# Optimization experiments

Measured on AMD Instinct MI355X. Metric: run time of the kernel, lower is better.

The kernel has to match this reference:

```python
import jax, jax.numpy as jnp
import numpy as np
import math

B, T, C, H, D = 2, 2048, 768, 12, 64


def _rms_norm(x):
    # torch F.rms_norm with eps=None -> finfo(dtype).eps, no learned weight
    eps = jnp.finfo(x.dtype).eps
    return x * jax.lax.rsqrt(jnp.mean(x * x, axis=-1, keepdims=True) + eps)


def _apply_rotary(x, cos, sin):
    # nanochat rotary: split head_dim into halves
    d = x.shape[-1] // 2
    x1, x2 = x[..., :d], x[..., d:]
    return jnp.concatenate([x1 * cos + x2 * sin, -x1 * sin + x2 * cos], axis=-1)


def setup_inputs() -> dict:
    key = jax.random.key(0)
    ks = jax.random.split(key, 8)
    s = 0.02
    x = jax.random.normal(ks[0], (B, T, C), jnp.float32)
    cos = jax.random.normal(ks[1], (1, T, 1, D // 2), jnp.float32)
    sin = jax.random.normal(ks[2], (1, T, 1, D // 2), jnp.float32)
    Wq = jax.random.normal(ks[3], (C, C), jnp.float32) * s
    Wk = jax.random.normal(ks[4], (C, C), jnp.float32) * s
    Wv = jax.random.normal(ks[5], (C, C), jnp.float32) * s
    Wo = jax.random.normal(ks[6], (C, C), jnp.float32) * s
    beta = jnp.ones((H,), jnp.float32) * 0.5
    return {"x": x, "cos": cos, "sin": sin, "Wq": Wq, "Wk": Wk, "Wv": Wv, "Wo": Wo, "beta": beta}


def reference(x, cos, sin, Wq, Wk, Wv, Wo, beta):
    b, t, c = x.shape
    h = beta.shape[0]
    d = c // h
    q = (x @ Wq.T).reshape(b, t, h, d)
    k = (x @ Wk.T).reshape(b, t, h, d)
    v = (x @ Wv.T).reshape(b, t, h, d)
    q = _rms_norm(_apply_rotary(q, cos, sin)).transpose(0, 2, 1, 3)  # (B,H,T,D)
    k = _rms_norm(_apply_rotary(k, cos, sin)).transpose(0, 2, 1, 3)
    v = v.transpose(0, 2, 1, 3)
    # phase coherence: mean over RoPE frequencies of cos(position_diff * theta)
    pos = jnp.arange(t, dtype=jnp.float32)
    theta = 10000.0 ** (-jnp.arange(0, d, 2, dtype=jnp.float32) / d)  # (D/2,)
    pdiff = pos[None, :] - pos[:, None]  # (T,T); cos is even so orientation is irrelevant
    coh_base = jnp.mean(jnp.cos(pdiff[:, :, None] * theta), axis=-1)  # (T,T)
    coherence = 1.0 + beta[None, :, None, None] * coh_base[None, None, :, :]  # (1,H,T,T)
    scores = jnp.einsum('bhqd,bhkd->bhqk', q, k) / math.sqrt(d)
    scores = scores * coherence
    w = jax.nn.softmax(scores, axis=-1)
    causal = jnp.tril(jnp.ones((t, t), dtype=bool))
    w = w * causal[None, None, :, :]
    w = w / (jnp.sum(w, axis=-1, keepdims=True) + 1e-8)
    y = jnp.einsum('bhqk,bhkd->bhqd', w, v)
    y = y.transpose(0, 2, 1, 3).reshape(b, t, c)
    return y @ Wo.T
```

## Files before the change

kernel.cpp:

```cpp
#include <hip/hip_runtime.h>
#include <hip/hip_bf16.h>
#include <math.h>

#define B_ 2
#define T_ 2048
#define C_ 768
#define H_ 12
#define D_ 64

typedef __attribute__((ext_vector_type(8))) short short8;
typedef __attribute__((ext_vector_type(4))) float f32x4;
typedef __attribute__((ext_vector_type(16))) float f32x16;

template <bool V> struct BoolC { static constexpr bool value = V; };

__device__ inline unsigned short f2bf(float f) {
    unsigned int x = __float_as_uint(f);
    unsigned int r = x + 0x7FFFu + ((x >> 16) & 1u);
    return (unsigned short)(r >> 16);
}

__device__ __forceinline__ unsigned cvtpk(float lo, float hi) {
    unsigned r;
    asm("v_cvt_pk_bf16_f32 %0, %1, %2" : "=v"(r) : "v"(lo), "v"(hi));
    return r;
}

__device__ __forceinline__ void plswap(unsigned& a, unsigned& b) {
    asm volatile("v_permlane32_swap_b32 %0, %1" : "+v"(a), "+v"(b));
}

__device__ __forceinline__ void gll16(const void* g, void* l) {
    __builtin_amdgcn_global_load_lds(
        (const __attribute__((address_space(1))) unsigned int*)g,
        (__attribute__((address_space(3))) unsigned int*)l, 16, 0, 0);
}

__global__ __launch_bounds__(256) void convert_all_kernel(const float* __restrict__ x,
                                                          const float* __restrict__ Wq,
                                                          const float* __restrict__ Wk,
                                                          const float* __restrict__ Wv,
                                                          const float* __restrict__ Wo,
                                                          unsigned short* __restrict__ xb,
                                                          unsigned short* __restrict__ wqkv,
                                                          unsigned short* __restrict__ wob,
                                                          float* __restrict__ coh) {
    if (blockIdx.x >= 5376) {
        int dd = (blockIdx.x - 5376) * 256 + threadIdx.x;
        if (dd < T_) {
            float s = 0.f;
            for (int m = 0; m < 32; ++m) {
                float theta = powf(10000.f, -(float)m / 32.f);
                s += cosf((float)dd * theta);
            }
            coh[dd] = s * (1.f / 32.f);
        }
        return;
    }
    int i = blockIdx.x * 256 + threadIdx.x;
    float4 v;
    ushort4* d;
    if (i < 786432) {
        v = ((const float4*)x)[i];
        d = (ushort4*)xb + i;
    } else {
        int wI = i - 786432;
        int widx = wI / 147456;
        int off = wI - widx * 147456;
        const float* W = widx == 0 ? Wq : widx == 1 ? Wk : widx == 2 ? Wv : Wo;
        v = ((const float4*)W)[off];
        unsigned short* base = (widx == 3) ? wob : (wqkv + widx * 589824);
        d = (ushort4*)base + off;
    }
    ushort4 o;
    o.x = f2bf(v.x); o.y = f2bf(v.y); o.z = f2bf(v.z); o.w = f2bf(v.w);
    *d = o;
}

__global__ __launch_bounds__(256) void gemm_qkv_kernel(const unsigned short* __restrict__ xb,
                                                       const unsigned short* __restrict__ wqkv,
                                                       const float* __restrict__ cosb,
                                                       const float* __restrict__ sinb,
                                                       unsigned short* __restrict__ qbf,
                                                       unsigned short* __restrict__ kbf,
                                                       unsigned short* __restrict__ vt) {
    __shared__ unsigned short lA[128][32];
    __shared__ unsigned short lB[128][32];
    __shared__ unsigned short tr[4][64][72];

    int bm = blockIdx.x, tn = blockIdx.y;
    int tid = threadIdx.x;
    int w = tid >> 6, lane = tid & 63;
    int rc = lane & 15, kg = lane >> 4;
    int wr = w >> 1, wc = w & 1;

    const unsigned short* ga = xb + (size_t)(bm * 128 + w * 32 + (lane >> 2)) * 768 + (lane & 3) * 8;
    const unsigned short* gb = wqkv + (size_t)(tn * 128 + w * 32 + (lane >> 2)) * 768 + (lane & 3) * 8;
    unsigned short* la0 = &lA[w * 32][0];
    unsigned short* la1 = &lA[w * 32 + 16][0];
    unsigned short* lb0 = &lB[w * 32][0];
    unsigned short* lb1 = &lB[w * 32 + 16][0];

    f32x4 acc[4][4];
    #pragma unroll
    for (int i = 0; i < 4; ++i)
        #pragma unroll
        for (int j = 0; j < 4; ++j) acc[i][j] = (f32x4){0.f, 0.f, 0.f, 0.f};

    for (int k0 = 0; k0 < 768; k0 += 32) {
        gll16(ga + k0, la0);
        gll16(ga + k0 + 16 * 768, la1);
        gll16(gb + k0, lb0);
        gll16(gb + k0 + 16 * 768, lb1);
        __syncthreads();
        short8 aF[4], bF[4];
        #pragma unroll
        for (int ai = 0; ai < 4; ++ai) aF[ai] = *(const short8*)&lA[wr * 64 + ai * 16 + rc][kg * 8];
        #pragma unroll
        for (int bj = 0; bj < 4; ++bj) bF[bj] = *(const short8*)&lB[wc * 64 + bj * 16 + rc][kg * 8];
        #pragma unroll
        for (int ai = 0; ai < 4; ++ai)
            #pragma unroll
            for (int bj = 0; bj < 4; ++bj)
                acc[ai][bj] = __builtin_amdgcn_mfma_f32_16x16x32_bf16(aF[ai], bF[bj], acc[ai][bj], 0, 0, 0);
        __syncthreads();
    }

    int hg = tn * 2 + wc;
    int tensor = hg / 12;
    int h = hg % 12;

    if (tensor < 2) {
        float scale = tensor == 0 ? 0.125f : 1.0f;
        unsigned short* dst = (tensor == 0 ? qbf : kbf);
        #pragma unroll
        for (int ai = 0; ai < 4; ++ai) {
            #pragma unroll
            for (int rr = 0; rr < 4; ++rr) {
                int m = bm * 128 + wr * 64 + ai * 16 + kg * 4 + rr;
                int b = m >> 11, t = m & 2047;
                float c0 = cosb[t * 32 + rc], c1 = cosb[t * 32 + 16 + rc];
                float s0 = sinb[t * 32 + rc], s1 = sinb[t * 32 + 16 + rc];
                float x0 = acc[ai][0][rr], x1 = acc[ai][1][rr];
                float x2 = acc[ai][2][rr], x3 = acc[ai][3][rr];
                float o0 = x0 * c0 + x2 * s0;
                float o1 = x1 * c1 + x3 * s1;
                float o2 = -x0 * s0 + x2 * c0;
                float o3 = -x1 * s1 + x3 * c1;
                float ss = o0 * o0 + o1 * o1 + o2 * o2 + o3 * o3;
                ss += __shfl_xor(ss, 1); ss += __shfl_xor(ss, 2);
                ss += __shfl_xor(ss, 4); ss += __shfl_xor(ss, 8);
                float rn = rsqrtf(ss * (1.f / 64.f) + 1.1920929e-07f) * scale;
                unsigned short* dp = dst + (((size_t)b * H_ + h) * T_ + t) * 64;
                dp[rc]      = f2bf(o0 * rn);
                dp[16 + rc] = f2bf(o1 * rn);
                dp[32 + rc] = f2bf(o2 * rn);
                dp[48 + rc] = f2bf(o3 * rn);
            }
        }
    } else {
        #pragma unroll
        for (int ai = 0; ai < 4; ++ai)
            #pragma unroll
            for (int bj = 0; bj < 4; ++bj)
                #pragma unroll
                for (int rr = 0; rr < 4; ++rr)
                    tr[w][bj * 16 + rc][ai * 16 + kg * 4 + rr] = f2bf(acc[ai][bj][rr]);
    }
    __syncthreads();
    if (tensor == 2) {
        int m0 = bm * 128 + wr * 64;
        int b = m0 >> 11, t0 = m0 & 2047;
        int d = lane;
        unsigned short* gp = vt + (((size_t)b * H_ + h) * 64 + d) * T_ + t0;
        const uint4* src = (const uint4*)&tr[w][d][0];
        #pragma unroll
        for (int i = 0; i < 8; ++i) ((uint4*)gp)[i] = src[i];
    }
}

__global__ __launch_bounds__(256) void gemm_out_kernel(const unsigned short* __restrict__ A,
                                                       const unsigned short* __restrict__ Bw,
                                                       float* __restrict__ C) {
    __shared__ unsigned short lA[128][32];
    __shared__ unsigned short lB[128][32];
    int bm = blockIdx.x, tn = blockIdx.y;
    int tid = threadIdx.x;
    int w = tid >> 6, lane = tid & 63;
    int rc = lane & 15, kg = lane >> 4;
    int wr = w >> 1, wc = w & 1;

    const unsigned short* ga = A + (size_t)(bm * 128 + w * 32 + (lane >> 2)) * 768 + (lane & 3) * 8;
    const unsigned short* gb = Bw + (size_t)(tn * 128 + w * 32 + (lane >> 2)) * 768 + (lane & 3) * 8;
    unsigned short* la0 = &lA[w * 32][0];
    unsigned short* la1 = &lA[w * 32 + 16][0];
    unsigned short* lb0 = &lB[w * 32][0];
    unsigned short* lb1 = &lB[w * 32 + 16][0];

    f32x4 acc[4][4];
    #pragma unroll
    for (int i = 0; i < 4; ++i)
        #pragma unroll
        for (int j = 0; j < 4; ++j) acc[i][j] = (f32x4){0.f, 0.f, 0.f, 0.f};

    for (int k0 = 0; k0 < 768; k0 += 32) {
        gll16(ga + k0, la0);
        gll16(ga + k0 + 16 * 768, la1);
        gll16(gb + k0, lb0);
        gll16(gb + k0 + 16 * 768, lb1);
        __syncthreads();
        short8 aF[4], bF[4];
        #pragma unroll
        for (int ai = 0; ai < 4; ++ai) aF[ai] = *(const short8*)&lA[wr * 64 + ai * 16 + rc][kg * 8];
        #pragma unroll
        for (int bj = 0; bj < 4; ++bj) bF[bj] = *(const short8*)&lB[wc * 64 + bj * 16 + rc][kg * 8];
        #pragma unroll
        for (int ai = 0; ai < 4; ++ai)
            #pragma unroll
            for (int bj = 0; bj < 4; ++bj)
                acc[ai][bj] = __builtin_amdgcn_mfma_f32_16x16x32_bf16(aF[ai], bF[bj], acc[ai][bj], 0, 0, 0);
        __syncthreads();
    }

    #pragma unroll
    for (int ai = 0; ai < 4; ++ai)
        #pragma unroll
        for (int rr = 0; rr < 4; ++rr) {
            int m = bm * 128 + wr * 64 + ai * 16 + kg * 4 + rr;
            #pragma unroll
            for (int bj = 0; bj < 4; ++bj)
                C[(size_t)m * 768 + tn * 128 + wc * 64 + bj * 16 + rc] = acc[ai][bj][rr];
        }
}

__global__ __launch_bounds__(256) void attn_flash_kernel(const unsigned short* __restrict__ qbf,
                                                         const unsigned short* __restrict__ kbf,
                                                         const unsigned short* __restrict__ vt,
                                                         const float* __restrict__ coh,
                                                         const float* __restrict__ beta,
                                                         unsigned short* __restrict__ yb) {
    __shared__ unsigned short kT[2][64][64];
    __shared__ unsigned short vT[2][64][64];
    __shared__ float cfl[T_];

    int p = blockIdx.x;
    int xcd = p & 7, kk = p >> 3;
    int bl = kk >> 5, jsl = kk & 31;
    int bh = xcd * 3 + bl;
    int jj = (bl == 0) ? jsl : (bl == 1 ? (31 - jsl) : ((jsl * 5 + 3) & 31));
    int tq = 31 - jj;
    int b = bh / H_, h = bh % H_;

    int tid = threadIdx.x;
    int w = tid >> 6, lane = tid & 63;
    int qs = w >> 1, js = w & 1;
    int ql = lane & 31, hl = lane >> 5;

    float bv = beta[h];
    for (int i = tid; i < T_; i += 256)
        cfl[i] = (1.f + bv * coh[i]) * 1.4426950408889634f;

    int qb = tq * 64;
    const unsigned short* kb = kbf + (size_t)bh * T_ * 64;
    const unsigned short* vb = vt + (size_t)bh * 64 * T_;

    const unsigned short* qrow = qbf + ((size_t)bh * T_ + qb + qs * 32 + ql) * 64 + hl * 8;
    short8 qf[4];
    #pragma unroll
    for (int d = 0; d < 4; ++d) qf[d] = *(const short8*)(qrow + d * 16);

    f32x16 acc0, acc1;
    #pragma unroll
    for (int i = 0; i < 16; ++i) { acc0[i] = 0.f; acc1[i] = 0.f; }
    float z = 0.f;

    int Rk = js * 32 + ql;
    int kby[4];
    #pragma unroll
    for (int d = 0; d < 4; ++d) kby[d] = Rk * 128 + (((d * 2 + hl) ^ (Rk & 7)) << 4);
    int vby0[2], vby1[2];
    #pragma unroll
    for (int ks = 0; ks < 2; ++ks) {
        int Rv0 = ql, Rv1 = 32 + ql;
        vby0[ks] = Rv0 * 128 + (((js * 4 + ks * 2 + hl) ^ (Rv0 & 7)) << 4);
        vby1[ks] = Rv1 * 128 + (((js * 4 + ks * 2 + hl) ^ (Rv1 & 7)) << 4);
    }
    const char* kbase = (const char*)&kT[0][0][0];
    const char* vbase = (const char*)&vT[0][0][0];

    int rloc = lane >> 3;
    int gsw = ((lane & 7) ^ rloc) * 8;
    int r0 = w * 16;

    auto stage = [&](int buf, int tj) {
        gll16(kb + (size_t)(tj + r0 + rloc) * 64 + gsw,      &kT[buf][r0][0]);
        gll16(kb + (size_t)(tj + r0 + 8 + rloc) * 64 + gsw,  &kT[buf][r0 + 8][0]);
        gll16(vb + (size_t)(r0 + rloc) * T_ + tj + gsw,      &vT[buf][r0][0]);
        gll16(vb + (size_t)(r0 + 8 + rloc) * T_ + tj + gsw,  &vT[buf][r0 + 8][0]);
    };

    int qpos = qb + qs * 32 + ql;

    auto body = [&](int buf, int tj, auto maskc) {
        constexpr bool M = decltype(maskc)::value;
        f32x16 s;
        #pragma unroll
        for (int i = 0; i < 16; ++i) s[i] = 0.f;
        const char* kp = kbase + buf * 8192;
        __builtin_amdgcn_s_setprio(1);
        #pragma unroll
        for (int d = 0; d < 4; ++d) {
            short8 kf = *(const short8*)(kp + kby[d]);
            s = __builtin_amdgcn_mfma_f32_32x32x16_bf16(kf, qf[d], s, 0, 0, 0);
        }
        __builtin_amdgcn_s_setprio(0);
        int base = qpos - tj - js * 32 - 4 * hl;
        float e[16];
        #pragma unroll
        for (int r = 0; r < 16; ++r) {
            int dd = base - ((r & 3) + 8 * (r >> 2));
            if constexpr (M) {
                float ex = __builtin_amdgcn_exp2f(s[r] * cfl[dd < 0 ? 0 : dd]);
                e[r] = dd >= 0 ? ex : 0.f;
            } else {
                e[r] = __builtin_amdgcn_exp2f(s[r] * cfl[dd]);
            }
            z += e[r];
        }
        unsigned A0 = cvtpk(e[0], e[1]),  B0 = cvtpk(e[2], e[3]);
        unsigned C0 = cvtpk(e[4], e[5]),  D0 = cvtpk(e[6], e[7]);
        unsigned E0 = cvtpk(e[8], e[9]),  F0 = cvtpk(e[10], e[11]);
        unsigned G0 = cvtpk(e[12], e[13]), H0 = cvtpk(e[14], e[15]);
        plswap(A0, C0); plswap(B0, D0); plswap(E0, G0); plswap(F0, H0);
        union U { unsigned u[4]; short8 s8; };
        U p0, p1;
        p0.u[0] = A0; p0.u[1] = B0; p0.u[2] = C0; p0.u[3] = D0;
        p1.u[0] = E0; p1.u[1] = F0; p1.u[2] = G0; p1.u[3] = H0;
        const char* vp = vbase + buf * 8192;
        short8 v00 = *(const short8*)(vp + vby0[0]);
        short8 v01 = *(const short8*)(vp + vby0[1]);
        short8 v10 = *(const short8*)(vp + vby1[0]);
        short8 v11 = *(const short8*)(vp + vby1[1]);
        __builtin_amdgcn_s_setprio(1);
        acc0 = __builtin_amdgcn_mfma_f32_32x32x16_bf16(v00, p0.s8, acc0, 0, 0, 0);
        acc0 = __builtin_amdgcn_mfma_f32_32x32x16_bf16(v01, p1.s8, acc0, 0, 0, 0);
        acc1 = __builtin_amdgcn_mfma_f32_32x32x16_bf16(v10, p0.s8, acc1, 0, 0, 0);
        acc1 = __builtin_amdgcn_mfma_f32_32x32x16_bf16(v11, p1.s8, acc1, 0, 0, 0);
        __builtin_amdgcn_s_setprio(0);
    };

    int nt = tq + 1;
    stage(0, 0);
    __syncthreads();
    int cur = 0;
    for (int it = 0; it < nt - 1; ++it) {
        stage(cur ^ 1, (it + 1) * 64);
        body(cur, it * 64, BoolC<false>{});
        __syncthreads();
        cur ^= 1;
    }
    if (qs > js)      body(cur, (nt - 1) * 64, BoolC<false>{});
    else if (qs == js) body(cur, (nt - 1) * 64, BoolC<true>{});
    __syncthreads();

    z += __shfl_xor(z, 32);
    float* osc = (float*)&kT[0][0][0];
    float* zbuf = (float*)&vT[0][0][0];
    if (js == 0) {
        float* o = osc + qs * 2048;
        #pragma unroll
        for (int r = 0; r < 16; ++r) {
            o[r * 64 + lane] = acc0[r];
            o[(16 + r) * 64 + lane] = acc1[r];
        }
        if (lane < 32) zbuf[qs * 32 + ql] = z;
    }
    __syncthreads();
    if (js == 1) {
        float zt = z + zbuf[qs * 32 + ql];
        float invz = 1.f / zt;
        const float* o = osc + qs * 2048;
        #pragma unroll
        for (int r = 0; r < 16; ++r) {
            acc0[r] = (acc0[r] + o[r * 64 + lane]) * invz;
            acc1[r] = (acc1[r] + o[(16 + r) * 64 + lane]) * invz;
        }
        int t = qb + qs * 32 + ql;
        unsigned short* yp = yb + (((size_t)b * T_ + t) * H_ + h) * 64;
        #pragma unroll
        for (int g = 0; g < 4; ++g) {
            uint2 st0, st1;
            st0.x = cvtpk(acc0[g * 4 + 0], acc0[g * 4 + 1]);
            st0.y = cvtpk(acc0[g * 4 + 2], acc0[g * 4 + 3]);
            *(uint2*)(yp + g * 8 + 4 * hl) = st0;
            st1.x = cvtpk(acc1[g * 4 + 0], acc1[g * 4 + 1]);
            st1.y = cvtpk(acc1[g * 4 + 2], acc1[g * 4 + 3]);
            *(uint2*)(yp + 32 + g * 8 + 4 * hl) = st1;
        }
    }
}

extern "C" void kernel_launch(void* const* d_in, const int* in_sizes, int n_in,
                              void* d_out, int out_size, void* d_ws, size_t ws_size,
                              hipStream_t stream) {
    const float* x    = (const float*)d_in[0];
    const float* cosb = (const float*)d_in[1];
    const float* sinb = (const float*)d_in[2];
    const float* Wq   = (const float*)d_in[3];
    const float* Wk   = (const float*)d_in[4];
    const float* Wv   = (const float*)d_in[5];
    const float* Wo   = (const float*)d_in[6];
    const float* beta = (const float*)d_in[7];
    float* out = (float*)d_out;

    char* ws = (char*)d_ws;
    unsigned short* xb   = (unsigned short*)(ws + 0);
    unsigned short* wqkv = (unsigned short*)(ws + 6291456);
    unsigned short* wob  = (unsigned short*)(ws + 9830400);
    unsigned short* qbf  = (unsigned short*)(ws + 11010048);
    unsigned short* kbf  = (unsigned short*)(ws + 17301504);
    unsigned short* vt   = (unsigned short*)(ws + 23592960);
    unsigned short* yb   = (unsigned short*)(ws + 29884416);
    float*          coh  = (float*)(ws + 36175872);

    convert_all_kernel<<<5384, 256, 0, stream>>>(x, Wq, Wk, Wv, Wo, xb, wqkv, wob, coh);

    dim3 gq(32, 18);
    gemm_qkv_kernel<<<gq, 256, 0, stream>>>(xb, wqkv, cosb, sinb, qbf, kbf, vt);

    attn_flash_kernel<<<B_ * H_ * (T_ / 64), 256, 0, stream>>>(qbf, kbf, vt, coh, beta, yb);

    dim3 go(32, 6);
    gemm_out_kernel<<<go, 256, 0, stream>>>(yb, wob, out);
}
```

Baseline: 114.9 us.

## Double-buffer GEMM LDS staging with vmcnt waits and narrow output GEMM tiles

Both projection GEMMs now double-buffer their LDS tiles. The next K-slice is issued before computing the current one, using explicit vmcnt waits and raw barriers instead of full __syncthreads. The QKV kernel puts the staging buffers and the transpose scratch in a union so LDS use stays bounded. The output GEMM switches to 128x64 tiles with twice as many blocks to raise occupancy on the small grid. The attention loop also replaces __syncthreads with a partial vmcnt wait plus barrier so prefetches stay in flight. The main risk is getting the waitcnt counts wrong for the async global-to-LDS loads.

```diff
diff --git a/kernel.cpp b/kernel.cpp
--- a/kernel.cpp
+++ b/kernel.cpp
@@ -13,6 +13,9 @@
 typedef __attribute__((ext_vector_type(16))) float f32x16;
 
 template <bool V> struct BoolC { static constexpr bool value = V; };
+
+#define SBAR() do { asm volatile("" ::: "memory"); __builtin_amdgcn_s_barrier(); asm volatile("" ::: "memory"); } while (0)
+#define WAITVM(N) asm volatile("s_waitcnt vmcnt(" #N ")" ::: "memory")
 
 __device__ inline unsigned short f2bf(float f) {
     unsigned int x = __float_as_uint(f);
@@ -77,6 +80,11 @@
     *d = o;
 }
 
+union QkvSmem {
+    struct { unsigned short A[2][128][32]; unsigned short Bm[2][128][32]; } g;
+    unsigned short tr[4][64][72];
+};
+
 __global__ __launch_bounds__(256) void gemm_qkv_kernel(const unsigned short* __restrict__ xb,
                                                        const unsigned short* __restrict__ wqkv,
                                                        const float* __restrict__ cosb,
@@ -84,9 +92,7 @@
                                                        unsigned short* __restrict__ qbf,
                                                        unsigned short* __restrict__ kbf,
                                                        unsigned short* __restrict__ vt) {
-    __shared__ unsigned short lA[128][32];
-    __shared__ unsigned short lB[128][32];
-    __shared__ unsigned short tr[4][64][72];
+    __shared__ QkvSmem sm;
 
     int bm = blockIdx.x, tn = blockIdx.y;
     int tid = threadIdx.x;
@@ -96,10 +102,6 @@
 
     const unsigned short* ga = xb + (size_t)(bm * 128 + w * 32 + (lane >> 2)) * 768 + (lane & 3) * 8;
     const unsigned short* gb = wqkv + (size_t)(tn * 128 + w * 32 + (lane >> 2)) * 768 + (lane & 3) * 8;
-    unsigned short* la0 = &lA[w * 32][0];
-    unsigned short* la1 = &lA[w * 32 + 16][0];
-    unsigned short* lb0 = &lB[w * 32][0];
-    unsigned short* lb1 = &lB[w * 32 + 16][0];
 
     f32x4 acc[4][4];
     #pragma unroll
@@ -107,24 +109,40 @@
         #pragma unroll
         for (int j = 0; j < 4; ++j) acc[i][j] = (f32x4){0.f, 0.f, 0.f, 0.f};
 
-    for (int k0 = 0; k0 < 768; k0 += 32) {
-        gll16(ga + k0, la0);
-        gll16(ga + k0 + 16 * 768, la1);
-        gll16(gb + k0, lb0);
-        gll16(gb + k0 + 16 * 768, lb1);
-        __syncthreads();
+    auto stageg = [&](int buf, int k0) {
+        gll16(ga + k0, &sm.g.A[buf][w * 32][0]);
+        gll16(ga + k0 + 16 * 768, &sm.g.A[buf][w * 32 + 16][0]);
+        gll16(gb + k0, &sm.g.Bm[buf][w * 32][0]);
+        gll16(gb + k0 + 16 * 768, &sm.g.Bm[buf][w * 32 + 16][0]);
+    };
+    auto comp = [&](int buf) {
         short8 aF[4], bF[4];
         #pragma unroll
-        for (int ai = 0; ai < 4; ++ai) aF[ai] = *(const short8*)&lA[wr * 64 + ai * 16 + rc][kg * 8];
-        #pragma unroll
-        for (int bj = 0; bj < 4; ++bj) bF[bj] = *(const short8*)&lB[wc * 64 + bj * 16 + rc][kg * 8];
+        for (int ai = 0; ai < 4; ++ai) aF[ai] = *(const short8*)&sm.g.A[buf][wr * 64 + ai * 16 + rc][kg * 8];
+        #pragma unroll
+        for (int bj = 0; bj < 4; ++bj) bF[bj] = *(const short8*)&sm.g.Bm[buf][wc * 64 + bj * 16 + rc][kg * 8];
+        __builtin_amdgcn_s_setprio(1);
         #pragma unroll
         for (int ai = 0; ai < 4; ++ai)
             #pragma unroll
             for (int bj = 0; bj < 4; ++bj)
                 acc[ai][bj] = __builtin_amdgcn_mfma_f32_16x16x32_bf16(aF[ai], bF[bj], acc[ai][bj], 0, 0, 0);
-        __syncthreads();
-    }
+        __builtin_amdgcn_s_setprio(0);
+    };
+
+    stageg(0, 0);
+    __syncthreads();
+    for (int kk = 0; kk < 23; ++kk) {
+        stageg((kk + 1) & 1, (kk + 1) * 32);
+        WAITVM(4);
+        SBAR();
+        comp(kk & 1);
+        SBAR();
+    }
+    WAITVM(0);
+    SBAR();
+    comp(1);
+    __syncthreads();
 
     int hg = tn * 2 + wc;
     int tensor = hg / 12;
@@ -165,7 +183,7 @@
             for (int bj = 0; bj < 4; ++bj)
                 #pragma unroll
                 for (int rr = 0; rr < 4; ++rr)
-                    tr[w][bj * 16 + rc][ai * 16 + kg * 4 + rr] = f2bf(acc[ai][bj][rr]);
+                    sm.tr[w][bj * 16 + rc][ai * 16 + kg * 4 + rr] = f2bf(acc[ai][bj][rr]);
     }
     __syncthreads();
     if (tensor == 2) {
@@ -173,7 +191,7 @@
         int b = m0 >> 11, t0 = m0 & 2047;
         int d = lane;
         unsigned short* gp = vt + (((size_t)b * H_ + h) * 64 + d) * T_ + t0;
-        const uint4* src = (const uint4*)&tr[w][d][0];
+        const uint4* src = (const uint4*)&sm.tr[w][d][0];
         #pragma unroll
         for (int i = 0; i < 8; ++i) ((uint4*)gp)[i] = src[i];
     }
@@ -182,8 +200,8 @@
 __global__ __launch_bounds__(256) void gemm_out_kernel(const unsigned short* __restrict__ A,
                                                        const unsigned short* __restrict__ Bw,
                                                        float* __restrict__ C) {
-    __shared__ unsigned short lA[128][32];
-    __shared__ unsigned short lB[128][32];
+    __shared__ unsigned short lA[2][128][32];
+    __shared__ unsigned short lB[2][64][32];
     int bm = blockIdx.x, tn = blockIdx.y;
     int tid = threadIdx.x;
     int w = tid >> 6, lane = tid & 63;
@@ -191,36 +209,46 @@
     int wr = w >> 1, wc = w & 1;
 
     const unsigned short* ga = A + (size_t)(bm * 128 + w * 32 + (lane >> 2)) * 768 + (lane & 3) * 8;
-    const unsigned short* gb = Bw + (size_t)(tn * 128 + w * 32 + (lane >> 2)) * 768 + (lane & 3) * 8;
-    unsigned short* la0 = &lA[w * 32][0];
-    unsigned short* la1 = &lA[w * 32 + 16][0];
-    unsigned short* lb0 = &lB[w * 32][0];
-    unsigned short* lb1 = &lB[w * 32 + 16][0];
-
-    f32x4 acc[4][4];
+    const unsigned short* gbB = Bw + (size_t)(tn * 64 + w * 16 + (lane >> 2)) * 768 + (lane & 3) * 8;
+
+    f32x4 acc[4][2];
     #pragma unroll
     for (int i = 0; i < 4; ++i)
         #pragma unroll
-        for (int j = 0; j < 4; ++j) acc[i][j] = (f32x4){0.f, 0.f, 0.f, 0.f};
-
-    for (int k0 = 0; k0 < 768; k0 += 32) {
-        gll16(ga + k0, la0);
-        gll16(ga + k0 + 16 * 768, la1);
-        gll16(gb + k0, lb0);
-        gll16(gb + k0 + 16 * 768, lb1);
-        __syncthreads();
-        short8 aF[4], bF[4];
-        #pragma unroll
-        for (int ai = 0; ai < 4; ++ai) aF[ai] = *(const short8*)&lA[wr * 64 + ai * 16 + rc][kg * 8];
-        #pragma unroll
-        for (int bj = 0; bj < 4; ++bj) bF[bj] = *(const short8*)&lB[wc * 64 + bj * 16 + rc][kg * 8];
+        for (int j = 0; j < 2; ++j) acc[i][j] = (f32x4){0.f, 0.f, 0.f, 0.f};
+
+    auto stageg = [&](int buf, int k0) {
+        gll16(ga + k0, &lA[buf][w * 32][0]);
+        gll16(ga + k0 + 16 * 768, &lA[buf][w * 32 + 16][0]);
+        gll16(gbB + k0, &lB[buf][w * 16][0]);
+    };
+    auto comp = [&](int buf) {
+        short8 aF[4], bF[2];
+        #pragma unroll
+        for (int ai = 0; ai < 4; ++ai) aF[ai] = *(const short8*)&lA[buf][wr * 64 + ai * 16 + rc][kg * 8];
+        #pragma unroll
+        for (int bj = 0; bj < 2; ++bj) bF[bj] = *(const short8*)&lB[buf][wc * 32 + bj * 16 + rc][kg * 8];
+        __builtin_amdgcn_s_setprio(1);
         #pragma unroll
         for (int ai = 0; ai < 4; ++ai)
             #pragma unroll
-            for (int bj = 0; bj < 4; ++bj)
+            for (int bj = 0; bj < 2; ++bj)
                 acc[ai][bj] = __builtin_amdgcn_mfma_f32_16x16x32_bf16(aF[ai], bF[bj], acc[ai][bj], 0, 0, 0);
-        __syncthreads();
-    }
+        __builtin_amdgcn_s_setprio(0);
+    };
+
+    stageg(0, 0);
+    __syncthreads();
+    for (int kk = 0; kk < 23; ++kk) {
+        stageg((kk + 1) & 1, (kk + 1) * 32);
+        WAITVM(3);
+        SBAR();
+        comp(kk & 1);
+        SBAR();
+    }
+    WAITVM(0);
+    SBAR();
+    comp(1);
 
     #pragma unroll
     for (int ai = 0; ai < 4; ++ai)
@@ -228,8 +256,8 @@
         for (int rr = 0; rr < 4; ++rr) {
             int m = bm * 128 + wr * 64 + ai * 16 + kg * 4 + rr;
             #pragma unroll
-            for (int bj = 0; bj < 4; ++bj)
-                C[(size_t)m * 768 + tn * 128 + wc * 64 + bj * 16 + rc] = acc[ai][bj][rr];
+            for (int bj = 0; bj < 2; ++bj)
+                C[(size_t)m * 768 + tn * 64 + wc * 32 + bj * 16 + rc] = acc[ai][bj][rr];
         }
 }
 
@@ -355,10 +383,14 @@
     int cur = 0;
     for (int it = 0; it < nt - 1; ++it) {
         stage(cur ^ 1, (it + 1) * 64);
+        WAITVM(4);
+        SBAR();
         body(cur, it * 64, BoolC<false>{});
-        __syncthreads();
+        SBAR();
         cur ^= 1;
     }
+    WAITVM(0);
+    SBAR();
     if (qs > js)      body(cur, (nt - 1) * 64, BoolC<false>{});
     else if (qs == js) body(cur, (nt - 1) * 64, BoolC<true>{});
     __syncthreads();
@@ -430,6 +462,6 @@
 
     attn_flash_kernel<<<B_ * H_ * (T_ / 64), 256, 0, stream>>>(qbf, kbf, vt, coh, beta, yb);
 
-    dim3 go(32, 6);
+    dim3 go(32, 12);
     gemm_out_kernel<<<go, 256, 0, stream>>>(yb, wob, out);
 }
```

New measurement: 106.4 us. 1.08x faster.
